# Performance work log

Hardware: AMD Instinct MI355X
Metric: run time of the kernel (lower is better)

## Reference

```python
import jax, jax.numpy as jnp
import numpy as np
from jax import lax

L, B, S, D, H = 4, 4, 2048, 1024, 2048
EPS = 1e-5


def setup_inputs() -> dict:
    key = jax.random.key(0)
    ks = jax.random.split(key, 8)

    def rn(k, shape, fan_in, fan_out):
        scale = (2.0 / (fan_in + fan_out)) ** 0.5  # xavier-ish
        return jax.random.normal(k, shape, jnp.float32) * scale

    return {
        "x": jax.random.normal(ks[0], (B, S, D), jnp.float32),
        "Wp1": rn(ks[1], (L, H, D), D, H),
        "bp1": jnp.zeros((L, H), jnp.float32),
        "Wp2": rn(ks[2], (L, H, D), D, H),
        "bp2": jnp.zeros((L, H), jnp.float32),
        "convW": rn(ks[3], (L, H, H, 3), 3 * H, H),  # torch Conv1d layout (O, I, K)
        "convb": jnp.zeros((L, H), jnp.float32),
        "Wz": rn(ks[4], (L, H, H), H, H),
        "bz": jnp.zeros((L, H), jnp.float32),
        "Wh": rn(ks[5], (L, H, H), H, H),
        "bh": jnp.zeros((L, H), jnp.float32),
        "Wd": rn(ks[6], (L, D, H), H, D),
        "bd": jnp.zeros((L, D), jnp.float32),
        # 4 LayerNorms per layer: [strand1_ln1, conv_ln, gru_ln, strand2_ln1]
        "ln_g": jnp.ones((L, 4, H), jnp.float32),
        "ln_b": jnp.zeros((L, 4, H), jnp.float32),
    }


def _ln(x, g, b):
    m = jnp.mean(x, axis=-1, keepdims=True)
    xc = x - m
    v = jnp.mean(xc * xc, axis=-1, keepdims=True)
    return xc * lax.rsqrt(v + EPS) * g + b


def _log_g(x):
    return jnp.where(x >= 0, jnp.log(jax.nn.relu(x) + 0.5), -jax.nn.softplus(-x))


def _min_gru(x, Wz, bz, Wh, bh):
    # x: (B, S, H); training-mode log-space parallel scan, h_0 = 0
    k = jnp.einsum('bsh,oh->bso', x, Wz) + bz
    log_z = -jax.nn.softplus(-k)
    log_coeffs = -jax.nn.softplus(k)
    log_h0 = jnp.full((x.shape[0], 1, Wz.shape[0]), jnp.log(0.5), x.dtype)  # log_g(0)
    log_tilde_h = _log_g(jnp.einsum('bsh,oh->bso', x, Wh) + bh)
    log_values = jnp.concatenate([log_h0, log_z + log_tilde_h], axis=1)  # (B,S+1,H)
    a_star = jnp.pad(jnp.cumsum(log_coeffs, axis=1), ((0, 0), (1, 0), (0, 0)))
    log_h = a_star + lax.cumlogsumexp(log_values - a_star, axis=1)
    return jnp.exp(log_h)[:, 1:]


def _conv1d(x, w, b):
    # x: (B, S, H) -> NCH conv with kernel 3, same padding
    y = lax.conv_general_dilated(
        x.transpose(0, 2, 1), w, window_strides=(1,), padding=((1, 1),),
        dimension_numbers=('NCH', 'OIH', 'NCH'))
    return (y + b[None, :, None]).transpose(0, 2, 1)


def _forward(x, Wp1, bp1, Wp2, bp2, convW, convb, Wz, bz, Wh, bh, Wd, bd, ln_g, ln_b):
    for i in range(L):
        s1 = _ln(jnp.einsum('bsd,hd->bsh', x, Wp1[i]) + bp1[i], ln_g[i, 0], ln_b[i, 0])
        s1 = _ln(_conv1d(s1, convW[i], convb[i]), ln_g[i, 1], ln_b[i, 1])
        s1 = jax.nn.silu(s1)
        s1 = _min_gru(s1, Wz[i], bz[i], Wh[i], bh[i])
        s1 = _ln(s1, ln_g[i, 2], ln_b[i, 2])
        s2 = jax.nn.silu(_ln(jnp.einsum('bsd,hd->bsh', x, Wp2[i]) + bp2[i], ln_g[i, 3], ln_b[i, 3]))
        x = jnp.einsum('bsh,dh->bsd', s1 * s2, Wd[i]) + bd[i] + x
    return x


def reference(x, Wp1, bp1, Wp2, bp2, convW, convb, Wz, bz, Wh, bh, Wd, bd, ln_g, ln_b):
    return _forward(x, Wp1, bp1, Wp2, bp2, convW, convb, Wz, bz, Wh, bh, Wd, bd, ln_g, ln_b)
```

## Files before the change

kernel.cpp:

```cpp
#include <hip/hip_runtime.h>

typedef unsigned short u16;
typedef short  s16x8 __attribute__((ext_vector_type(8)));
typedef float  f32x4 __attribute__((ext_vector_type(4)));
typedef unsigned short u16x4 __attribute__((ext_vector_type(4)));

#define LDS_AS __attribute__((address_space(3)))
#define GLB_AS __attribute__((address_space(1)))

__device__ __forceinline__ float bf2f(u16 x) {
    unsigned u = ((unsigned)x) << 16;
    return __builtin_bit_cast(float, u);
}
__device__ __forceinline__ u16 f2bf(float f) {
    unsigned u = __builtin_bit_cast(unsigned, f);
    return (u16)((u + 0x7FFFu + ((u >> 16) & 1u)) >> 16);
}
__device__ __forceinline__ void gload16(const u16* g, u16* l) {
    __builtin_amdgcn_global_load_lds((const GLB_AS unsigned int*)g,
                                     (LDS_AS unsigned int*)l, 16, 0, 0);
}

static constexpr int Lc = 4, Sc = 2048, Dc = 1024, Hc = 2048, Mc = 8192;
static constexpr int CH = 64, CL = 32;
static constexpr int NCHAN = 4 * Hc;
static constexpr int KPW = 4096;

#define BAR() __builtin_amdgcn_s_barrier()
#define VMCNT(n) asm volatile("s_waitcnt vmcnt(" #n ")" ::: "memory")

#define READ_A(d, BUF, MH)                                                     \
    _Pragma("unroll") for (int mf = 0; mf < 4; ++mf) {                         \
        d[mf][0] = *(const s16x8*)(aB0 + (BUF)*16384 + (MH)*4096 + mf*1024);   \
        d[mf][1] = *(const s16x8*)(aB1 + (BUF)*16384 + (MH)*4096 + mf*1024);   \
    }
#define READ_B(BUF, NH)                                                        \
    _Pragma("unroll") for (int jb = 0; jb < 2; ++jb) {                         \
        bq[jb][0] = *(const s16x8*)(bB0 + (BUF)*16384 + (NH)*2048 + jb*1024);  \
        bq[jb][1] = *(const s16x8*)(bB1 + (BUF)*16384 + (NH)*2048 + jb*1024);  \
    }
#define QUAD(a, MH, NH)                                                        \
    _Pragma("unroll") for (int mf = 0; mf < 4; ++mf)                           \
    _Pragma("unroll") for (int jb = 0; jb < 2; ++jb)                           \
    _Pragma("unroll") for (int kk = 0; kk < 2; ++kk)                           \
        acc[(MH)*4 + mf][(NH)*2 + jb] = __builtin_amdgcn_mfma_f32_16x16x32_bf16( \
            a[mf][kk], bq[jb][kk], acc[(MH)*4 + mf][(NH)*2 + jb], 0, 0, 0);

#define STAGE_A(BUF, H, KT) {                                                  \
    if (CONV) {                                                                \
        const int seg_ = ((KT)*64) >> 11;                                      \
        const int kb_  = ((KT)*64) & (Hc - 1);                                 \
        const int r0_  = convRow + (H)*128 + seg_;                             \
        const u16* s0_ = ((unsigned)(r0_ - bb) < (unsigned)Sc)                 \
                             ? A + (size_t)r0_ * lda + kb_ + scol : zerobuf;   \
        const u16* s1_ = ((unsigned)(r0_ + 8 - bb) < (unsigned)Sc)             \
                             ? A + (size_t)(r0_ + 8) * lda + kb_ + scol : zerobuf; \
        gload16(s0_, ldsA + (BUF)*16384 + (H)*8192);                           \
        gload16(s1_, ldsA + (BUF)*16384 + (H)*8192 + 512);                     \
    } else {                                                                   \
        const u16* s_ = srcA + (size_t)((H)*128) * lda + (KT)*64;              \
        gload16(s_,                   ldsA + (BUF)*16384 + (H)*8192);          \
        gload16(s_ + 8*(size_t)lda,   ldsA + (BUF)*16384 + (H)*8192 + 512);    \
    } }
#define STAGE_B(BUF, H, KT) {                                                  \
    const u16* s_ = srcB + (size_t)((H)*128) * K + (KT)*64;                    \
    gload16(s_,                 ldsB + (BUF)*16384 + (H)*8192);                \
    gload16(s_ + 8*(size_t)K,   ldsB + (BUF)*16384 + (H)*8192 + 512);          \
}

template <int CONV, int EPI>
__global__ __launch_bounds__(512, 2)
void gemm8(const u16* __restrict__ A, const u16* __restrict__ Bw,
           const float* __restrict__ bias, u16* __restrict__ Cb,
           float* __restrict__ Cf, const float* __restrict__ resid,
           u16* __restrict__ xout,
           int M, int N, int K, int lda, const u16* __restrict__ zerobuf) {
    (void)M;
    __shared__ __align__(16) u16 As[2][256][64];
    __shared__ __align__(16) u16 Bs[2][256][64];

    const int tid = threadIdx.x;
    const int w = tid >> 6, l = tid & 63;
    const int wm = w & 1, wn = w >> 1;

    const unsigned nwg = gridDim.x * gridDim.y;
    unsigned id = blockIdx.x + gridDim.x * blockIdx.y;
    id = (id & 7u) * (nwg >> 3) + (id >> 3);
    const int bx = (int)(id % gridDim.x);
    const int by = (int)(id / gridDim.x);
    const int rowBase = by * 256;
    const int colBase = bx * 256;

    const int srow = w * 16 + (l >> 3);
    const int scol = ((l & 7) ^ (l >> 3)) << 3;
    const u16* srcB = Bw + (size_t)(colBase + srow) * K + scol;
    const u16* srcA = A + (size_t)(rowBase + srow) * lda + scol;
    u16* const ldsA = &As[0][0][0] + w * 1024;
    u16* const ldsB = &Bs[0][0][0] + w * 1024;
    const int bb = rowBase & ~(Sc - 1);
    const int convRow = rowBase + srow - 1;

    const int r16 = l & 15, slot = l >> 4;
    const int swz = (r16 & 7) << 4;
    const int co0 = (((slot << 4)      ) ^ swz) >> 1;
    const int co1 = (((slot << 4) | 64 ) ^ swz) >> 1;
    const u16* aB0 = &As[0][0][0] + (wm * 128 + r16) * 64 + co0;
    const u16* aB1 = &As[0][0][0] + (wm * 128 + r16) * 64 + co1;
    const u16* bB0 = &Bs[0][0][0] + (wn * 64  + r16) * 64 + co0;
    const u16* bB1 = &Bs[0][0][0] + (wn * 64  + r16) * 64 + co1;

    f32x4 acc[8][4];
#pragma unroll
    for (int m = 0; m < 8; ++m)
#pragma unroll
        for (int n = 0; n < 4; ++n)
#pragma unroll
            for (int r = 0; r < 4; ++r) acc[m][n][r] = 0.f;

    s16x8 a0[4][2], a1[4][2], bq[2][2];

    STAGE_A(0, 0, 0); STAGE_A(0, 1, 0); STAGE_B(0, 0, 0); STAGE_B(0, 1, 0);
    VMCNT(4);
    STAGE_A(1, 0, 1); STAGE_A(1, 1, 1); STAGE_B(1, 0, 1);
    VMCNT(6);
    BAR();

    const int NI = K >> 7;
    for (int i = 0; i < NI; ++i) {
        const int t1 = 2 * i + 1, t2 = 2 * i + 2, t3 = 2 * i + 3;
        const bool more = (i + 1 < NI);
        READ_A(a0, 0, 0); READ_B(0, 0);
        STAGE_B(1, 1, t1);
        BAR();
        __builtin_amdgcn_s_setprio(1); QUAD(a0, 0, 0); __builtin_amdgcn_s_setprio(0);
        BAR();
        READ_A(a1, 0, 1);
        BAR();
        __builtin_amdgcn_s_setprio(1); QUAD(a1, 1, 0); __builtin_amdgcn_s_setprio(0);
        BAR();
        READ_B(0, 1);
        if (more) { STAGE_A(0, 0, t2); STAGE_A(0, 1, t2); }
        BAR();
        __builtin_amdgcn_s_setprio(1); QUAD(a0, 0, 1); __builtin_amdgcn_s_setprio(0);
        BAR();
        if (more) STAGE_B(0, 0, t2);
        BAR();
        __builtin_amdgcn_s_setprio(1); QUAD(a1, 1, 1); __builtin_amdgcn_s_setprio(0);
        if (more) { VMCNT(6); } else { VMCNT(0); }
        BAR();
        READ_A(a0, 1, 0); READ_B(1, 0);
        if (more) STAGE_B(0, 1, t2);
        BAR();
        __builtin_amdgcn_s_setprio(1); QUAD(a0, 0, 0); __builtin_amdgcn_s_setprio(0);
        BAR();
        READ_A(a1, 1, 1);
        BAR();
        __builtin_amdgcn_s_setprio(1); QUAD(a1, 1, 0); __builtin_amdgcn_s_setprio(0);
        BAR();
        READ_B(1, 1);
        if (more) { STAGE_A(1, 0, t3); STAGE_A(1, 1, t3); }
        BAR();
        __builtin_amdgcn_s_setprio(1); QUAD(a0, 0, 1); __builtin_amdgcn_s_setprio(0);
        BAR();
        if (more) STAGE_B(1, 0, t3);
        BAR();
        __builtin_amdgcn_s_setprio(1); QUAD(a1, 1, 1); __builtin_amdgcn_s_setprio(0);
        if (more) VMCNT(6);
        BAR();
    }

    const int coll  = colBase + wn * 64 + r16;
    const int row00 = rowBase + wm * 128 + slot * 4;
#pragma unroll
    for (int m8 = 0; m8 < 8; ++m8) {
#pragma unroll
        for (int n4 = 0; n4 < 4; ++n4) {
            const int col = coll + n4 * 16;
            const float bv = bias[col];
            const int row0 = row00 + m8 * 16;
#pragma unroll
            for (int r = 0; r < 4; ++r) {
                const size_t idx = (size_t)(row0 + r) * N + col;
                float v = acc[m8][n4][r] + bv;
                if (EPI == 0) {
                    Cb[idx] = f2bf(v);
                } else {
                    v += resid[idx];
                    Cf[idx]   = v;
                    xout[idx] = f2bf(v);
                }
            }
        }
    }
}

__global__ __launch_bounds__(256)
void ln_fuse(const u16* __restrict__ in, u16* __restrict__ out,
             const float* __restrict__ g, const float* __restrict__ b,
             const u16* __restrict__ mul, int do_silu) {
    __shared__ float sred[4], qred[4];
    const int row = blockIdx.x, tid = threadIdx.x;
    const int lane = tid & 63, wave = tid >> 6;
    const size_t base = (size_t)row * Hc + tid * 8;

    s16x8 v8 = *(const s16x8*)(in + base);
    float x[8];
#pragma unroll
    for (int j = 0; j < 8; j++) x[j] = bf2f((u16)v8[j]);
    float s = 0.f, q = 0.f;
#pragma unroll
    for (int j = 0; j < 8; j++) { s += x[j]; q += x[j] * x[j]; }
#pragma unroll
    for (int off = 32; off > 0; off >>= 1) {
        s += __shfl_down(s, off);
        q += __shfl_down(q, off);
    }
    if (lane == 0) { sred[wave] = s; qred[wave] = q; }
    __syncthreads();
    const float St = sred[0] + sred[1] + sred[2] + sred[3];
    const float Qt = qred[0] + qred[1] + qred[2] + qred[3];
    const float mean = St * (1.0f / Hc);
    const float var  = Qt * (1.0f / Hc) - mean * mean;
    const float rs   = rsqrtf(var + 1e-5f);

    const int c = tid * 8;
    const float4 g0 = *(const float4*)(g + c), g1 = *(const float4*)(g + c + 4);
    const float4 b0 = *(const float4*)(b + c), b1 = *(const float4*)(b + c + 4);
    const float gg[8] = {g0.x, g0.y, g0.z, g0.w, g1.x, g1.y, g1.z, g1.w};
    const float bb[8] = {b0.x, b0.y, b0.z, b0.w, b1.x, b1.y, b1.z, b1.w};
    s16x8 m8;
    if (mul) m8 = *(const s16x8*)(mul + base);
    s16x8 o8;
#pragma unroll
    for (int j = 0; j < 8; j++) {
        float y = (x[j] - mean) * rs * gg[j] + bb[j];
        if (do_silu) y = y / (1.0f + __expf(-y));
        if (mul) y *= bf2f((u16)m8[j]);
        o8[j] = (short)f2bf(y);
    }
    *(s16x8*)(out + base) = o8;
}

__device__ __forceinline__ void scan_step(float k, float p, float& ct, float& vt) {
    const float l1p = __logf(1.f + __expf(-fabsf(k)));
    ct = -(fmaxf(k, 0.f) + l1p);
    const float lg = (p >= 0.f) ? __logf(p + 0.5f)
                                : -(fmaxf(-p, 0.f) + __logf(1.f + __expf(-fabsf(p))));
    vt = -(fmaxf(-k, 0.f) + l1p) + lg;
}
__device__ __forceinline__ float laddexp(float a, float b) {
    const float m = fmaxf(a, b);
    return m + __logf(1.f + __expf(-fabsf(a - b)));
}

__global__ __launch_bounds__(256)
void scan_part1(const u16* __restrict__ kp,
                float* __restrict__ Cc, float* __restrict__ Vv) {
    const int tid = threadIdx.x;
    const int hb = blockIdx.x & 7;
    const int c  = (blockIdx.x >> 3) & 63;
    const int b  = blockIdx.x >> 9;
    const int h  = hb * 256 + tid;
    size_t idx = (size_t)(b * Sc + c * CL) * KPW + h;
    float C = 0.f, V = -1e30f;
#pragma unroll 4
    for (int t = 0; t < CL; t++) {
        float ct, vt;
        scan_step(bf2f(kp[idx]), bf2f(kp[idx + Hc]), ct, vt);
        V = laddexp(V + ct, vt);
        C += ct;
        idx += KPW;
    }
    const int chan = b * Hc + h;
    Cc[c * NCHAN + chan] = C;
    Vv[c * NCHAN + chan] = V;
}

__global__ __launch_bounds__(256)
void scan_mid(const float* __restrict__ Cc, const float* __restrict__ Vv,
              float* __restrict__ carry) {
    const int chan = blockIdx.x * 256 + threadIdx.x;
    float lh = -0.69314718f;
    for (int c = 0; c < CH; c++) {
        carry[c * NCHAN + chan] = lh;
        lh = laddexp(lh + Cc[c * NCHAN + chan], Vv[c * NCHAN + chan]);
    }
}

__global__ __launch_bounds__(256)
void scan_part3(const u16* __restrict__ kp,
                const float* __restrict__ carry, u16* __restrict__ out) {
    const int tid = threadIdx.x;
    const int hb = blockIdx.x & 7;
    const int c  = (blockIdx.x >> 3) & 63;
    const int b  = blockIdx.x >> 9;
    const int h  = hb * 256 + tid;
    size_t idx = (size_t)(b * Sc + c * CL) * KPW + h;
    size_t odx = (size_t)(b * Sc + c * CL) * Hc + h;
    float lh = carry[c * NCHAN + (b * Hc + h)];
#pragma unroll 4
    for (int t = 0; t < CL; t++) {
        float ct, vt;
        scan_step(bf2f(kp[idx]), bf2f(kp[idx + Hc]), ct, vt);
        lh = laddexp(lh + ct, vt);
        out[odx] = f2bf(__expf(lh));
        idx += KPW;
        odx += Hc;
    }
}

__global__ __launch_bounds__(256)
void castf2b(const float* __restrict__ in, u16* __restrict__ out, int n) {
    const int i = (blockIdx.x * 256 + threadIdx.x) << 2;
    if (i >= n) return;
    const float4 v = *(const float4*)(in + i);
    u16x4 o;
    o.x = f2bf(v.x); o.y = f2bf(v.y); o.z = f2bf(v.z); o.w = f2bf(v.w);
    *(u16x4*)(out + i) = o;
}

__global__ __launch_bounds__(256)
void conv_tr(const float* __restrict__ w, u16* __restrict__ out) {
    const int idx = blockIdx.x * 256 + threadIdx.x;
    const float* src = w + (size_t)idx * 3;
    const float a = src[0], b = src[1], c = src[2];
    const int o = idx >> 11, ii = idx & (Hc - 1);
    u16* dst = out + (size_t)o * (3 * Hc) + ii;
    dst[0]        = f2bf(a);
    dst[Hc]       = f2bf(b);
    dst[2 * Hc]   = f2bf(c);
}

static inline void launch_gemm8(int conv, int epi,
                                const u16* A, const u16* Bw, const float* bias,
                                u16* Cb, float* Cf, const float* resid, u16* xout,
                                int M, int N, int K, int lda,
                                const u16* zero, hipStream_t s) {
    dim3 grid(N / 256, M / 256), blk(512);
    if (conv)
        gemm8<1, 0><<<grid, blk, 0, s>>>(A, Bw, bias, Cb, Cf, resid, xout, M, N, K, lda, zero);
    else if (epi)
        gemm8<0, 1><<<grid, blk, 0, s>>>(A, Bw, bias, Cb, Cf, resid, xout, M, N, K, lda, zero);
    else
        gemm8<0, 0><<<grid, blk, 0, s>>>(A, Bw, bias, Cb, Cf, resid, xout, M, N, K, lda, zero);
}

extern "C" void kernel_launch(void* const* d_in, const int* in_sizes, int n_in,
                              void* d_out, int out_size, void* d_ws, size_t ws_size,
                              hipStream_t stream) {
    (void)in_sizes; (void)n_in; (void)out_size; (void)ws_size;
    const float* x0    = (const float*)d_in[0];
    const float* Wp1   = (const float*)d_in[1];
    const float* bp1   = (const float*)d_in[2];
    const float* Wp2   = (const float*)d_in[3];
    const float* bp2   = (const float*)d_in[4];
    const float* convW = (const float*)d_in[5];
    const float* convb = (const float*)d_in[6];
    const float* Wz    = (const float*)d_in[7];
    const float* bz    = (const float*)d_in[8];
    const float* Wh    = (const float*)d_in[9];
    const float* bh    = (const float*)d_in[10];
    const float* Wd    = (const float*)d_in[11];
    const float* bd    = (const float*)d_in[12];
    const float* lng   = (const float*)d_in[13];
    const float* lnb   = (const float*)d_in[14];
    float* out = (float*)d_out;

    char* ws = (char*)d_ws;
    u16* wbuf = (u16*)(ws);
    u16* s1   = (u16*)(ws + 25165824);
    u16* t1   = (u16*)(ws + 58720256);
    u16* kp   = (u16*)(ws + 92274688);
    u16* s2   = kp;
    u16* xb   = (u16*)(ws + 159383552);
    u16* zero = (u16*)(ws + 176160768);
    float* scanC = (float*)(ws + 176161792);
    float* scanV = (float*)(ws + 178258944);
    float* carry = (float*)(ws + 180356096);
    float* bias2 = (float*)(ws + 182453248);

    hipMemsetAsync(zero, 0, 1024, stream);
    castf2b<<<dim3((Mc * Dc / 4) / 256), dim3(256), 0, stream>>>(x0, xb, Mc * Dc);

    const size_t wpStride = (size_t)Hc * Dc;
    const size_t cvStride = (size_t)Hc * Hc * 3;
    const size_t wzStride = (size_t)Hc * Hc;
    const size_t wdStride = (size_t)Dc * Hc;

    for (int i = 0; i < Lc; ++i) {
        const float* g0 = lng + ((size_t)i * 4 + 0) * Hc; const float* be0 = lnb + ((size_t)i * 4 + 0) * Hc;
        const float* g1 = lng + ((size_t)i * 4 + 1) * Hc; const float* be1 = lnb + ((size_t)i * 4 + 1) * Hc;
        const float* g2 = lng + ((size_t)i * 4 + 2) * Hc; const float* be2 = lnb + ((size_t)i * 4 + 2) * Hc;
        const float* g3 = lng + ((size_t)i * 4 + 3) * Hc; const float* be3 = lnb + ((size_t)i * 4 + 3) * Hc;

        castf2b<<<dim3((int)(wpStride / 4 / 256)), dim3(256), 0, stream>>>(Wp1 + i * wpStride, wbuf, (int)wpStride);
        launch_gemm8(0, 0, xb, wbuf, bp1 + (size_t)i * Hc, t1, nullptr, nullptr, nullptr,
                     Mc, Hc, Dc, Dc, zero, stream);
        ln_fuse<<<dim3(Mc), dim3(256), 0, stream>>>(t1, s1, g0, be0, nullptr, 0);

        conv_tr<<<dim3((Hc * Hc) / 256), dim3(256), 0, stream>>>(convW + i * cvStride, wbuf);
        launch_gemm8(1, 0, s1, wbuf, convb + (size_t)i * Hc, t1, nullptr, nullptr, nullptr,
                     Mc, Hc, 3 * Hc, Hc, zero, stream);
        ln_fuse<<<dim3(Mc), dim3(256), 0, stream>>>(t1, s1, g1, be1, nullptr, 1);

        castf2b<<<dim3((int)(wzStride / 4 / 256)), dim3(256), 0, stream>>>(Wz + i * wzStride, wbuf, (int)wzStride);
        castf2b<<<dim3((int)(wzStride / 4 / 256)), dim3(256), 0, stream>>>(Wh + i * wzStride, wbuf + wzStride, (int)wzStride);
        hipMemcpyAsync(bias2,        bz + (size_t)i * Hc, Hc * sizeof(float), hipMemcpyDeviceToDevice, stream);
        hipMemcpyAsync(bias2 + Hc,   bh + (size_t)i * Hc, Hc * sizeof(float), hipMemcpyDeviceToDevice, stream);
        launch_gemm8(0, 0, s1, wbuf, bias2, kp, nullptr, nullptr, nullptr,
                     Mc, KPW, Hc, Hc, zero, stream);
        scan_part1<<<dim3(2048), dim3(256), 0, stream>>>(kp, scanC, scanV);
        scan_mid<<<dim3(32), dim3(256), 0, stream>>>(scanC, scanV, carry);
        scan_part3<<<dim3(2048), dim3(256), 0, stream>>>(kp, carry, t1);
        ln_fuse<<<dim3(Mc), dim3(256), 0, stream>>>(t1, s1, g2, be2, nullptr, 0);

        castf2b<<<dim3((int)(wpStride / 4 / 256)), dim3(256), 0, stream>>>(Wp2 + i * wpStride, wbuf, (int)wpStride);
        launch_gemm8(0, 0, xb, wbuf, bp2 + (size_t)i * Hc, t1, nullptr, nullptr, nullptr,
                     Mc, Hc, Dc, Dc, zero, stream);
        ln_fuse<<<dim3(Mc), dim3(256), 0, stream>>>(t1, s2, g3, be3, s1, 1);

        castf2b<<<dim3((int)(wdStride / 4 / 256)), dim3(256), 0, stream>>>(Wd + i * wdStride, wbuf, (int)wdStride);
        launch_gemm8(0, 1, s2, wbuf, bd + (size_t)i * Dc, nullptr, out,
                     (i == 0) ? x0 : out, xb, Mc, Dc, Hc, Hc, zero, stream);
    }
}
```

Before: 2.942 ms.

## Fuse Wp1/Wp2 projections into one GEMM, add LDS waits, batch scan loads

When workspace is large enough, the two input projections are run as one N=4096 GEMM into a wide buffer, and the LayerNorm kernels read it with a stride, so xb is read once instead of twice. A prep2 kernel casts two weight matrices and copies the concatenated biases in a single launch, replacing separate casts and memcpys. The GEMM main loop gains explicit lgkmcnt waits and scheduling barriers around the MFMA quads. scan_mid now loads eight chunks ahead before its serial recurrence. The fused path depends on ws_size and needs an extra 64MB buffer.

After: 2.923 ms. About the same (-0.6%).

```diff
diff --git a/kernel.cpp b/kernel.cpp
--- a/kernel.cpp
+++ b/kernel.cpp
@@ -28,6 +28,12 @@
 
 #define BAR() __builtin_amdgcn_s_barrier()
 #define VMCNT(n) asm volatile("s_waitcnt vmcnt(" #n ")" ::: "memory")
+#define LGK8() asm volatile("s_waitcnt lgkmcnt(8)" ::: "memory")
+#define WAIT0()                                                                \
+    do {                                                                       \
+        asm volatile("s_waitcnt lgkmcnt(0)" ::: "memory");                     \
+        __builtin_amdgcn_sched_barrier(0);                                     \
+    } while (0)
 
 #define READ_A(d, BUF, MH)                                                     \
     _Pragma("unroll") for (int mf = 0; mf < 4; ++mf) {                         \
@@ -131,16 +137,17 @@
         const bool more = (i + 1 < NI);
         READ_A(a0, 0, 0); READ_B(0, 0);
         STAGE_B(1, 1, t1);
-        BAR();
+        LGK8();
+        BAR(); WAIT0();
         __builtin_amdgcn_s_setprio(1); QUAD(a0, 0, 0); __builtin_amdgcn_s_setprio(0);
         BAR();
         READ_A(a1, 0, 1);
-        BAR();
+        BAR(); WAIT0();
         __builtin_amdgcn_s_setprio(1); QUAD(a1, 1, 0); __builtin_amdgcn_s_setprio(0);
         BAR();
         READ_B(0, 1);
         if (more) { STAGE_A(0, 0, t2); STAGE_A(0, 1, t2); }
-        BAR();
+        BAR(); WAIT0();
         __builtin_amdgcn_s_setprio(1); QUAD(a0, 0, 1); __builtin_amdgcn_s_setprio(0);
         BAR();
         if (more) STAGE_B(0, 0, t2);
@@ -150,16 +157,17 @@
         BAR();
         READ_A(a0, 1, 0); READ_B(1, 0);
         if (more) STAGE_B(0, 1, t2);
-        BAR();
+        LGK8();
+        BAR(); WAIT0();
         __builtin_amdgcn_s_setprio(1); QUAD(a0, 0, 0); __builtin_amdgcn_s_setprio(0);
         BAR();
         READ_A(a1, 1, 1);
-        BAR();
+        BAR(); WAIT0();
         __builtin_amdgcn_s_setprio(1); QUAD(a1, 1, 0); __builtin_amdgcn_s_setprio(0);
         BAR();
         READ_B(1, 1);
         if (more) { STAGE_A(1, 0, t3); STAGE_A(1, 1, t3); }
-        BAR();
+        BAR(); WAIT0();
         __builtin_amdgcn_s_setprio(1); QUAD(a0, 0, 1); __builtin_amdgcn_s_setprio(0);
         BAR();
         if (more) STAGE_B(1, 0, t3);
@@ -195,15 +203,16 @@
 }
 
 __global__ __launch_bounds__(256)
-void ln_fuse(const u16* __restrict__ in, u16* __restrict__ out,
+void ln_fuse(const u16* __restrict__ in, int instride, u16* __restrict__ out,
              const float* __restrict__ g, const float* __restrict__ b,
              const u16* __restrict__ mul, int do_silu) {
     __shared__ float sred[4], qred[4];
     const int row = blockIdx.x, tid = threadIdx.x;
     const int lane = tid & 63, wave = tid >> 6;
-    const size_t base = (size_t)row * Hc + tid * 8;
-
-    s16x8 v8 = *(const s16x8*)(in + base);
+    const size_t ibase = (size_t)row * instride + tid * 8;
+    const size_t obase = (size_t)row * Hc + tid * 8;
+
+    s16x8 v8 = *(const s16x8*)(in + ibase);
     float x[8];
 #pragma unroll
     for (int j = 0; j < 8; j++) x[j] = bf2f((u16)v8[j]);
@@ -229,7 +238,7 @@
     const float gg[8] = {g0.x, g0.y, g0.z, g0.w, g1.x, g1.y, g1.z, g1.w};
     const float bb[8] = {b0.x, b0.y, b0.z, b0.w, b1.x, b1.y, b1.z, b1.w};
     s16x8 m8;
-    if (mul) m8 = *(const s16x8*)(mul + base);
+    if (mul) m8 = *(const s16x8*)(mul + obase);
     s16x8 o8;
 #pragma unroll
     for (int j = 0; j < 8; j++) {
@@ -238,7 +247,7 @@
         if (mul) y *= bf2f((u16)m8[j]);
         o8[j] = (short)f2bf(y);
     }
-    *(s16x8*)(out + base) = o8;
+    *(s16x8*)(out + obase) = o8;
 }
 
 __device__ __forceinline__ void scan_step(float k, float p, float& ct, float& vt) {
@@ -281,9 +290,18 @@
               float* __restrict__ carry) {
     const int chan = blockIdx.x * 256 + threadIdx.x;
     float lh = -0.69314718f;
-    for (int c = 0; c < CH; c++) {
-        carry[c * NCHAN + chan] = lh;
-        lh = laddexp(lh + Cc[c * NCHAN + chan], Vv[c * NCHAN + chan]);
+    for (int cb = 0; cb < CH; cb += 8) {
+        float Cr[8], Vr[8];
+#pragma unroll
+        for (int j = 0; j < 8; j++) {
+            Cr[j] = Cc[(cb + j) * NCHAN + chan];
+            Vr[j] = Vv[(cb + j) * NCHAN + chan];
+        }
+#pragma unroll
+        for (int j = 0; j < 8; j++) {
+            carry[(cb + j) * NCHAN + chan] = lh;
+            lh = laddexp(lh + Cr[j], Vr[j]);
+        }
     }
 }
 
@@ -320,6 +338,27 @@
 }
 
 __global__ __launch_bounds__(256)
+void prep2(const float* __restrict__ srcA, const float* __restrict__ srcB,
+           const float* __restrict__ bA, const float* __restrict__ bB,
+           u16* __restrict__ dst, float* __restrict__ bias_dst, int nPerHalf) {
+    const int bid = blockIdx.x, tid = threadIdx.x;
+    const int halfBlocks = gridDim.x >> 1;
+    const int half = (bid >= halfBlocks) ? 1 : 0;
+    const size_t i = ((size_t)(bid - half * halfBlocks) * 256 + tid) * 4;
+    const float* src = half ? srcB : srcA;
+    const float4 v = *(const float4*)(src + i);
+    u16x4 o;
+    o.x = f2bf(v.x); o.y = f2bf(v.y); o.z = f2bf(v.z); o.w = f2bf(v.w);
+    *(u16x4*)(dst + (size_t)half * nPerHalf + i) = o;
+    if (bid < 4) {
+        const int j = bid * 1024 + tid * 4;
+        const float4 vb = (j < 2048) ? *(const float4*)(bA + j)
+                                     : *(const float4*)(bB + (j - 2048));
+        *(float4*)(bias_dst + j) = vb;
+    }
+}
+
+__global__ __launch_bounds__(256)
 void conv_tr(const float* __restrict__ w, u16* __restrict__ out) {
     const int idx = blockIdx.x * 256 + threadIdx.x;
     const float* src = w + (size_t)idx * 3;
@@ -348,7 +387,7 @@
 extern "C" void kernel_launch(void* const* d_in, const int* in_sizes, int n_in,
                               void* d_out, int out_size, void* d_ws, size_t ws_size,
                               hipStream_t stream) {
-    (void)in_sizes; (void)n_in; (void)out_size; (void)ws_size;
+    (void)in_sizes; (void)n_in; (void)out_size;
     const float* x0    = (const float*)d_in[0];
     const float* Wp1   = (const float*)d_in[1];
     const float* bp1   = (const float*)d_in[2];
@@ -378,6 +417,8 @@
     float* scanV = (float*)(ws + 178258944);
     float* carry = (float*)(ws + 180356096);
     float* bias2 = (float*)(ws + 182453248);
+    u16* P       = (u16*)(ws + 184549376);
+    const bool FUSEP = ws_size >= 251658240ull;
 
     hipMemsetAsync(zero, 0, 1024, stream);
     castf2b<<<dim3((Mc * Dc / 4) / 256), dim3(256), 0, stream>>>(x0, xb, Mc * Dc);
@@ -393,34 +434,48 @@
         const float* g2 = lng + ((size_t)i * 4 + 2) * Hc; const float* be2 = lnb + ((size_t)i * 4 + 2) * Hc;
         const float* g3 = lng + ((size_t)i * 4 + 3) * Hc; const float* be3 = lnb + ((size_t)i * 4 + 3) * Hc;
 
-        castf2b<<<dim3((int)(wpStride / 4 / 256)), dim3(256), 0, stream>>>(Wp1 + i * wpStride, wbuf, (int)wpStride);
-        launch_gemm8(0, 0, xb, wbuf, bp1 + (size_t)i * Hc, t1, nullptr, nullptr, nullptr,
-                     Mc, Hc, Dc, Dc, zero, stream);
-        ln_fuse<<<dim3(Mc), dim3(256), 0, stream>>>(t1, s1, g0, be0, nullptr, 0);
+        if (FUSEP) {
+            prep2<<<dim3(2 * (int)(wpStride / 1024)), dim3(256), 0, stream>>>(
+                Wp1 + i * wpStride, Wp2 + i * wpStride,
+                bp1 + (size_t)i * Hc, bp2 + (size_t)i * Hc, wbuf, bias2, (int)wpStride);
+            launch_gemm8(0, 0, xb, wbuf, bias2, P, nullptr, nullptr, nullptr,
+                         Mc, KPW, Dc, Dc, zero, stream);
+            ln_fuse<<<dim3(Mc), dim3(256), 0, stream>>>(P, KPW, s1, g0, be0, nullptr, 0);
+        } else {
+            castf2b<<<dim3((int)(wpStride / 4 / 256)), dim3(256), 0, stream>>>(Wp1 + i * wpStride, wbuf, (int)wpStride);
+            launch_gemm8(0, 0, xb, wbuf, bp1 + (size_t)i * Hc, t1, nullptr, nullptr, nullptr,
+                         Mc, Hc, Dc, Dc, zero, stream);
+            ln_fuse<<<dim3(Mc), dim3(256), 0, stream>>>(t1, Hc, s1, g0, be0, nullptr, 0);
+        }
 
         conv_tr<<<dim3((Hc * Hc) / 256), dim3(256), 0, stream>>>(convW + i * cvStride, wbuf);
         launch_gemm8(1, 0, s1, wbuf, convb + (size_t)i * Hc, t1, nullptr, nullptr, nullptr,
                      Mc, Hc, 3 * Hc, Hc, zero, stream);
-        ln_fuse<<<dim3(Mc), dim3(256), 0, stream>>>(t1, s1, g1, be1, nullptr, 1);
-
-        castf2b<<<dim3((int)(wzStride / 4 / 256)), dim3(256), 0, stream>>>(Wz + i * wzStride, wbuf, (int)wzStride);
-        castf2b<<<dim3((int)(wzStride / 4 / 256)), dim3(256), 0, stream>>>(Wh + i * wzStride, wbuf + wzStride, (int)wzStride);
-        hipMemcpyAsync(bias2,        bz + (size_t)i * Hc, Hc * sizeof(float), hipMemcpyDeviceToDevice, stream);
-        hipMemcpyAsync(bias2 + Hc,   bh + (size_t)i * Hc, Hc * sizeof(float), hipMemcpyDeviceToDevice, stream);
+        ln_fuse<<<dim3(Mc), dim3(256), 0, stream>>>(t1, Hc, s1, g1, be1, nullptr, 1);
+
+        prep2<<<dim3(2 * (int)(wzStride / 1024)), dim3(256), 0, stream>>>(
+            Wz + i * wzStride, Wh + i * wzStride,
+            bz + (size_t)i * Hc, bh + (size_t)i * Hc, wbuf, bias2, (int)wzStride);
         launch_gemm8(0, 0, s1, wbuf, bias2, kp, nullptr, nullptr, nullptr,
                      Mc, KPW, Hc, Hc, zero, stream);
         scan_part1<<<dim3(2048), dim3(256), 0, stream>>>(kp, scanC, scanV);
         scan_mid<<<dim3(32), dim3(256), 0, stream>>>(scanC, scanV, carry);
         scan_part3<<<dim3(2048), dim3(256), 0, stream>>>(kp, carry, t1);
-        ln_fuse<<<dim3(Mc), dim3(256), 0, stream>>>(t1, s1, g2, be2, nullptr, 0);
-
-        castf2b<<<dim3((int)(wpStride / 4 / 256)), dim3(256), 0, stream>>>(Wp2 + i * wpStride, wbuf, (int)wpStride);
-        launch_gemm8(0, 0, xb, wbuf, bp2 + (size_t)i * Hc, t1, nullptr, nullptr, nullptr,
-                     Mc, Hc, Dc, Dc, zero, stream);
-        ln_fuse<<<dim3(Mc), dim3(256), 0, stream>>>(t1, s2, g3, be3, s1, 1);
-
-        castf2b<<<dim3((int)(wdStride / 4 / 256)), dim3(256), 0, stream>>>(Wd + i * wdStride, wbuf, (int)wdStride);
-        launch_gemm8(0, 1, s2, wbuf, bd + (size_t)i * Dc, nullptr, out,
-                     (i == 0) ? x0 : out, xb, Mc, Dc, Hc, Hc, zero, stream);
-    }
-}
+        ln_fuse<<<dim3(Mc), dim3(256), 0, stream>>>(t1, Hc, s1, g2, be2, nullptr, 0);
+
+        if (FUSEP) {
+            ln_fuse<<<dim3(Mc), dim3(256), 0, stream>>>(P + Hc, KPW, t1, g3, be3, s1, 1);
+            castf2b<<<dim3((int)(wdStride / 4 / 256)), dim3(256), 0, stream>>>(Wd + i * wdStride, wbuf, (int)wdStride);
+            launch_gemm8(0, 1, t1, wbuf, bd + (size_t)i * Dc, nullptr, out,
+                         (i == 0) ? x0 : out, xb, Mc, Dc, Hc, Hc, zero, stream);
+        } else {
+            castf2b<<<dim3((int)(wpStride / 4 / 256)), dim3(256), 0, stream>>>(Wp2 + i * wpStride, wbuf, (int)wpStride);
+            launch_gemm8(0, 0, xb, wbuf, bp2 + (size_t)i * Hc, t1, nullptr, nullptr, nullptr,
+                         Mc, Hc, Dc, Dc, zero, stream);
+            ln_fuse<<<dim3(Mc), dim3(256), 0, stream>>>(t1, Hc, s2, g3, be3, s1, 1);
+            castf2b<<<dim3((int)(wdStride / 4 / 256)), dim3(256), 0, stream>>>(Wd + i * wdStride, wbuf, (int)wdStride);
+            launch_gemm8(0, 1, s2, wbuf, bd + (size_t)i * Dc, nullptr, out,
+                         (i == 0) ? x0 : out, xb, Mc, Dc, Hc, Hc, zero, stream);
+        }
+    }
+}
```
